# Optimization experiments

Measured on AMD Instinct MI355X. Metric: run time of the kernel, lower is better.

The kernel has to match this reference:

```python
import jax, jax.numpy as jnp
import numpy as np

STRIDE = 16
SIZES = np.array([128.0, 256.0, 512.0], np.float32)
RATIOS = np.array([0.5, 1.0, 2.0], np.float32)
N_POS, N_NEG = 32, 32          # n_sample=64, pos_ratio=0.5
POS_THR, NEG_THR = 0.7, 0.2
W_CONF, W_REG = 1.0, 5.0


def _conv(x, w, b, stride, pad):
    y = jax.lax.conv_general_dilated(x, w, (stride, stride), [(pad, pad), (pad, pad)],
                                     dimension_numbers=('NCHW', 'OIHW', 'NCHW'))
    return y + b[None, :, None, None]


def _anchors(fw, fh, stride):
    # 9 anchors per center: 3 sizes x 3 aspect ratios
    ws = (SIZES[:, None] * np.sqrt(RATIOS)[None, :]).reshape(-1)
    hs = (SIZES[:, None] / np.sqrt(RATIOS)[None, :]).reshape(-1)
    wh = jnp.asarray(np.stack([ws, hs], -1))                      # (9,2)
    cx = (jnp.arange(fw, dtype=jnp.float32) + 0.5) * stride
    cy = (jnp.arange(fh, dtype=jnp.float32) + 0.5) * stride
    gx, gy = jnp.meshgrid(cx, cy, indexing='ij')                  # x-major, like the torch list comp
    ctr = jnp.stack([gx, gy], -1)[:, :, None, :]                  # (fw,fh,1,2)
    tl = ctr - wh / 2.0
    xywh = jnp.concatenate([tl, jnp.broadcast_to(wh, tl.shape)], -1)  # (fw,fh,9,4)
    return xywh.reshape(-1, 4)


def _xywh_to_xyxy(b):
    return jnp.concatenate([b[:, :2], b[:, :2] + b[:, 2:]], -1)


def _iou(a, b):  # a [N,4], b [M,4], xyxy
    lt = jnp.maximum(a[:, None, :2], b[None, :, :2])
    rb = jnp.minimum(a[:, None, 2:], b[None, :, 2:])
    inter = jnp.clip(rb - lt, 0.0).prod(-1)
    aa = (a[:, 2] - a[:, 0]) * (a[:, 3] - a[:, 1])
    ab = (b[:, 2] - b[:, 0]) * (b[:, 3] - b[:, 1])
    return inter / (aa[:, None] + ab[None, :] - inter)


def _head_flat(y, per):  # [1, 9*per, H, W] -> [W*H*9, per], matching anchor flatten order
    _, _, H, W = y.shape
    return y[0].reshape(9, per, H, W).transpose(3, 2, 0, 1).reshape(-1, per)


def _apply_offsets(boxes, off):  # decode proposals from xyxy boxes + (dx,dy,dw,dh)
    w = boxes[:, 2] - boxes[:, 0]; h = boxes[:, 3] - boxes[:, 1]
    cx = boxes[:, 0] + 0.5 * w;    cy = boxes[:, 1] + 0.5 * h
    ncx = cx + off[:, 0] * w;      ncy = cy + off[:, 1] * h
    nw = w * jnp.exp(off[:, 2]);   nh = h * jnp.exp(off[:, 3])
    return jnp.stack([ncx - nw / 2, ncy - nh / 2, ncx + nw / 2, ncy + nh / 2], -1)


def _box_offset(anc, gt):
    aw = anc[:, 2] - anc[:, 0]; ah = anc[:, 3] - anc[:, 1]
    acx = anc[:, 0] + 0.5 * aw; acy = anc[:, 1] + 0.5 * ah
    gw = gt[:, 2] - gt[:, 0];   gh = gt[:, 3] - gt[:, 1]
    gcx = gt[:, 0] + 0.5 * gw;  gcy = gt[:, 1] + 0.5 * gh
    return jnp.stack([(gcx - acx) / aw, (gcy - acy) / ah,
                      jnp.log(gw / aw), jnp.log(gh / ah)], -1)


def setup_inputs():
    key = jax.random.key(0)
    ks = jax.random.split(key, 12)
    img_data = jax.random.normal(ks[0], (1, 3, 1600, 1600), jnp.float32)
    x1 = jax.random.uniform(ks[1], (64,), minval=0.0, maxval=1400.0)
    y1 = jax.random.uniform(ks[2], (64,), minval=0.0, maxval=1400.0)
    bw = jax.random.uniform(ks[3], (64,), minval=32.0, maxval=200.0)
    bh = jax.random.uniform(ks[4], (64,), minval=32.0, maxval=200.0)
    gt_boxes = jnp.stack([x1, y1, x1 + bw, y1 + bh], -1)[None]   # [1,64,4], all valid (no -1 pad)
    gt_classes = jax.random.randint(ks[5], (1, 64), 1, 21, jnp.int32)
    def w(k, shape, fan):
        return jax.random.normal(k, shape, jnp.float32) * np.float32(np.sqrt(2.0 / fan))
    return dict(
        img_data=img_data, gt_boxes=gt_boxes, gt_classes=gt_classes,
        w1=w(ks[6], (64, 3, 7, 7), 3 * 49),      b1=jnp.zeros(64, jnp.float32),
        w2=w(ks[7], (256, 64, 3, 3), 64 * 9),    b2=jnp.zeros(256, jnp.float32),
        w_rpn=w(ks[8], (256, 256, 3, 3), 256 * 9), b_rpn=jnp.zeros(256, jnp.float32),
        w_cls=w(ks[9], (18, 256, 1, 1), 256),    b_cls=jnp.zeros(18, jnp.float32),
        w_reg=w(ks[10], (36, 256, 1, 1), 256),   b_reg=jnp.zeros(36, jnp.float32),
    )


def reference(img_data, gt_boxes, gt_classes, w1, b1, w2, b2, w_rpn, b_rpn, w_cls, b_cls, w_reg, b_reg):
    # --- feature extractor (total stride 16) ---
    fm = jax.nn.relu(_conv(img_data, w1, b1, 4, 3))
    fm = jax.nn.relu(_conv(fm, w2, b2, 4, 1))            # [1,256,100,100]
    H, W = fm.shape[2], fm.shape[3]
    # --- anchors + IoU matching ---
    anchors_xywh = _anchors(W, H, STRIDE)                # [N,4] xywh
    anchors_xyxy = _xywh_to_xyxy(anchors_xywh)
    gt = gt_boxes[0]                                     # [M,4], all valid
    ious = _iou(anchors_xyxy, gt)                        # [N,M]
    N = ious.shape[0]
    gt_max = ious.max(0)                                 # best iou per gt
    is_gt_best = (ious == gt_max[None, :]).any(1)        # torch: where(iou == gt_max)[0]
    anc_argmax = ious.argmax(1)
    anc_max = ious.max(1)
    labels = jnp.full((N,), -1.0, jnp.float32)
    labels = jnp.where(anc_max < NEG_THR, 0.0, labels)
    labels = jnp.where(is_gt_best, 1.0, labels)
    labels = jnp.where(anc_max > POS_THR, 1.0, labels)
    # --- deterministic pos/neg sampling (fixed sizes; replaces randperm subsampling) ---
    idx = jnp.arange(N, dtype=jnp.float32)
    _, pos_index = jax.lax.top_k(jnp.where(labels == 1.0, anc_max, -1.0), N_POS)
    _, neg_index = jax.lax.top_k(jnp.where(labels == 0.0, 1e6 - idx, -1e9), N_NEG)
    bboxes_pos = anchors_xyxy[pos_index]                 # box_convert(xywh->xyxy) of pos anchors
    # --- proposal module (RPN head) ---
    h = jax.nn.relu(_conv(fm, w_rpn, b_rpn, 1, 1))
    cls = _head_flat(_conv(h, w_cls, b_cls, 1, 0), 2)    # [N,2]
    reg = _head_flat(_conv(h, w_reg, b_reg, 1, 0), 4)    # [N,4]
    pos_score = cls[pos_index]
    neg_score = cls[neg_index]
    offset_pos = reg[pos_index]
    proposals = _apply_offsets(bboxes_pos, offset_pos)
    # --- losses ---
    gt_offset = _box_offset(bboxes_pos, gt[anc_argmax[pos_index]])
    logits = jnp.concatenate([pos_score, neg_score], 0)  # [64,2]
    tgt = jnp.concatenate([jnp.ones(N_POS, jnp.int32), jnp.zeros(N_NEG, jnp.int32)])
    logp = jax.nn.log_softmax(logits, -1)
    cls_loss = -logp[jnp.arange(N_POS + N_NEG), tgt].mean()
    d = gt_offset - offset_pos
    ad = jnp.abs(d)
    reg_loss = jnp.where(ad < 1.0, 0.5 * d * d, ad - 0.5).mean()
    total_rpn_loss = W_CONF * cls_loss + W_REG * reg_loss
    gt_cls_pos = gt_classes[0][anc_argmax[pos_index]]
    return (total_rpn_loss, fm, proposals, pos_index, gt_cls_pos)
```

## Files before the change

### kernel.cpp

```cpp
#include <hip/hip_runtime.h>
#include <math.h>


#define CAP 4096

typedef __attribute__((ext_vector_type(8))) short bf16x8;
typedef __attribute__((ext_vector_type(4))) float f32x4;

#define OFF_F1T     0
#define OFF_HBUF    0
#define OFF_FMT     5171328
#define OFF_CPART   6503040
#define OFF_RPART   7223040
#define OFF_WA1     8663040
#define OFF_W9_2    8672448
#define OFF_W9_3    8746176
#define OFF_WTC     9041088
#define OFF_WTG     9045696
#define OFF_AARG    9054912
#define OFF_NEGM    9144912
#define OFF_POSM    9147728
#define OFF_GTMAX   9150544
#define OFF_CANDS   9150688
#define OFF_CANDI   9154784

__device__ __forceinline__ unsigned short f2bf(float f) {
    unsigned int u = __float_as_uint(f);
    u += 0x7fffu + ((u >> 16) & 1u);
    return (unsigned short)(u >> 16);
}

__device__ __forceinline__ void anchor_box(int i, float& x0, float& y0,
                                           float& x1, float& y1, float& area) {
#pragma clang fp contract(off)
    const float sizes[3]  = {128.f, 256.f, 512.f};
    const float ratios[3] = {0.5f, 1.f, 2.f};
    int a = i % 9;
    int q = i / 9;
    int iy = q % 100;
    int ix = q / 100;
    int s = a / 3, r = a % 3;
    float sq = sqrtf(ratios[r]);
    float w = sizes[s] * sq;
    float h = sizes[s] / sq;
    float cx = ((float)ix + 0.5f) * 16.0f;
    float cy = ((float)iy + 0.5f) * 16.0f;
    x0 = cx - w * 0.5f;
    y0 = cy - h * 0.5f;
    x1 = x0 + w;
    y1 = y0 + h;
    area = (x1 - x0) * (y1 - y0);
}

__device__ __forceinline__ float iou_one(float ax0, float ay0, float ax1, float ay1, float aa,
                                         float bx0, float by0, float bx1, float by1, float ab) {
#pragma clang fp contract(off)
    float ltx = fmaxf(ax0, bx0), lty = fmaxf(ay0, by0);
    float rbx = fminf(ax1, bx1), rby = fminf(ay1, by1);
    float iw = fmaxf(rbx - ltx, 0.0f);
    float ih = fmaxf(rby - lty, 0.0f);
    float inter = iw * ih;
    return inter / ((aa + ab) - inter);
}

__global__ __launch_bounds__(256) void setup_kernel(const float* __restrict__ wc, float* __restrict__ wtc,
                                                    const float* __restrict__ wg, float* __restrict__ wtg,
                                                    const float* __restrict__ w1, unsigned short* __restrict__ wa1,
                                                    const float* __restrict__ w2, unsigned short* __restrict__ w9_2,
                                                    const float* __restrict__ wr, unsigned short* __restrict__ w9_3,
                                                    unsigned int* __restrict__ f1t_u, unsigned int* __restrict__ fmt_u,
                                                    unsigned int* __restrict__ gtmax) {
    int i = blockIdx.x * 256 + threadIdx.x;
    if (i < 65) { gtmax[i] = 0u; return; }
    i -= 65;
    if (i < 103040) {
        if (i < 51328) {
            int p = i >> 5, part = i & 31;
            int x, y;
            if (p < 804) { y = (p < 402) ? 0 : 401; x = p % 402; }
            else { int j = p - 804; x = (j < 400) ? 0 : 401; y = 1 + (j % 400); }
            f1t_u[(y * 402 + x) * 32 + part] = 0u;
        } else {
            int i2 = i - 51328;
            int p = i2 >> 7, part = i2 & 127;
            int x, y;
            if (p < 204) { y = (p < 102) ? 0 : 101; x = p % 102; }
            else { int j = p - 204; x = (j < 100) ? 0 : 101; y = 1 + (j % 100); }
            fmt_u[(y * 102 + x) * 128 + part] = 0u;
        }
        return;
    }
    i -= 103040;
    if (i < 4608) { int c = i / 256, k = i - c * 256; wtc[k * 18 + c] = wc[i]; return; }
    i -= 4608;
    if (i < 9216) { int c = i / 256, k = i - c * 256; wtg[k * 36 + c] = wg[i]; return; }
    i -= 9216;
    if (i < 12288) {
        int oc = i / 192, k = i - oc * 192;
        int q = k >> 3, kx = k & 7;
        int ky = q / 3, ic = q - (q / 3) * 3;
        wa1[i] = (q < 21 && kx < 7) ? f2bf(w1[oc * 147 + ic * 49 + ky * 7 + kx])
                                    : (unsigned short)0;
        return;
    }
    i -= 12288;
    if (i < 147456) {
        int cc = i >> 14;
        int rem = i & 16383;
        int ocT = rem >> 10;
        int rem2 = rem & 1023;
        int kcl = rem2 >> 9;
        int lane = (rem2 & 511) >> 3;
        int e = rem2 & 7;
        int oc = ocT * 16 + (lane & 15);
        int ic = kcl * 32 + (lane >> 4) * 8 + e;
        w9_2[i] = f2bf(w2[(oc * 64 + ic) * 9 + cc]);
        return;
    }
    i -= 147456;
    if (i < 589824) {
        int cc = i >> 14;
        int rem = i & 16383;
        int ocT = rem >> 10;
        int rem2 = rem & 1023;
        int kcl = rem2 >> 9;
        int lane = (rem2 & 511) >> 3;
        int e = rem2 & 7;
        int kk = cc >> 2, chv = cc & 3;
        int oc = ocT * 16 + (lane & 15);
        int icl = kcl * 32 + (lane >> 4) * 8 + e;
        w9_3[i] = f2bf(wr[(oc * 256 + chv * 64 + icl) * 9 + kk]);
    }
}

__global__ __launch_bounds__(256) void conv1_mfma(const float* __restrict__ img,
                                                  const unsigned short* __restrict__ wA,
                                                  const float* __restrict__ bias,
                                                  unsigned short* __restrict__ f1t) {
    __shared__ unsigned short win[24 * 260];
    __shared__ unsigned short tileT[64 * 72];
    int t = threadIdx.x;
    int wave = t >> 6, lane = t & 63;
    int quad = lane >> 4, l16 = lane & 15;
    int oy = blockIdx.y;
    int ox0 = blockIdx.x * 64;
    int gx0 = ox0 * 4 - 3;
    int gy0 = 4 * oy - 3;

    int gx = gx0 + t;
    bool xok = (gx >= 0) && (gx < 1600);
    float v[21];
#pragma unroll
    for (int r = 0; r < 21; r++) {
        int ky = r / 3, ic = r - (r / 3) * 3;
        int gy = gy0 + ky;
        v[r] = (xok && gy >= 0 && gy < 1600) ? img[(ic * 1600 + gy) * 1600 + gx] : 0.f;
    }
    float vt = 0.f;
    int rt = t >> 2, ctl = 256 + (t & 3);
    if (rt < 21) {
        int ky = rt / 3, ic = rt - (rt / 3) * 3;
        int gy = gy0 + ky;
        int gxt = gx0 + ctl;
        vt = (gxt >= 0 && gxt < 1600 && gy >= 0 && gy < 1600)
                 ? img[(ic * 1600 + gy) * 1600 + gxt] : 0.f;
    }
    bf16x8 afr[6];
    {
        const bf16x8* ap = (const bf16x8*)(wA + (wave * 16 + l16) * 192 + quad * 8);
#pragma unroll
        for (int c = 0; c < 6; c++) afr[c] = ap[c * 4];
    }
#pragma unroll
    for (int r = 0; r < 21; r++) win[r * 260 + t] = f2bf(v[r]);
    if (rt < 21) win[rt * 260 + ctl] = f2bf(vt);
    win[5460 + t] = 0;
    win[5460 + 256 + t] = 0;
    win[5460 + 512 + t] = 0;
    if (t < 12) win[5460 + 768 + t] = 0;
    __syncthreads();

    f32x4 acc[4];
#pragma unroll
    for (int j = 0; j < 4; j++) acc[j] = (f32x4){0.f, 0.f, 0.f, 0.f};
#pragma unroll
    for (int ch = 0; ch < 6; ch++) {
        const unsigned short* wrow = win + (ch * 4 + quad) * 260;
#pragma unroll
        for (int j = 0; j < 4; j++) {
            int px = j * 16 + l16;
            const unsigned long long* bp = (const unsigned long long*)(wrow + 4 * px);
            union { unsigned long long u[2]; bf16x8 v; } uu;
            uu.u[0] = bp[0];
            uu.u[1] = bp[1];
            acc[j] = __builtin_amdgcn_mfma_f32_16x16x32_bf16(afr[ch], uu.v, acc[j], 0, 0, 0);
        }
    }
#pragma unroll
    for (int reg = 0; reg < 4; reg++) {
        int oc = wave * 16 + quad * 4 + reg;
        float bv = bias[oc];
#pragma unroll
        for (int j = 0; j < 4; j++) {
            int px = j * 16 + l16;
            tileT[px * 72 + oc] = f2bf(fmaxf(acc[j][reg] + bv, 0.f));
        }
    }
    __syncthreads();
    int px = t >> 2, part = t & 3;
    int ox = ox0 + px;
    if (ox < 400) {
        int row = (oy + 1) * 402 + ox + 1;
        uint4 v0 = *(const uint4*)(tileT + px * 72 + part * 16);
        uint4 v1 = *(const uint4*)(tileT + px * 72 + part * 16 + 8);
        *(uint4*)(f1t + row * 64 + part * 16) = v0;
        *(uint4*)(f1t + row * 64 + part * 16 + 8) = v1;
    }
}

template<int ICC, int RS, int S, bool WRT>
__global__ __launch_bounds__(512, 4) void conv_gemm(const unsigned short* __restrict__ Bt,
                                                    const unsigned short* __restrict__ A9,
                                                    const float* __restrict__ bias,
                                                    float* __restrict__ outF,
                                                    unsigned short* __restrict__ outT) {
    const int NC = ICC / 64;
    const int HC = S * 24 + 3;
    const int LROW = ICC + 8;
    const int CHW = ICC / 8;
    const int TOT = 3 * HC * CHW;
    const int NIT = (TOT + 511) / 512;
    __shared__ __align__(16) unsigned short blds[3 * HC * LROW];
    int t = threadIdx.x;
    int xs = blockIdx.x, y = blockIdx.y;

    uint4 stg[NIT];
#pragma unroll
    for (int i = 0; i < NIT; i++) {
        int idx = t + i * 512;
        if (idx < TOT) {
            int row = idx / CHW, e = idx - row * CHW;
            int ky = row / HC, c = row - ky * HC;
            stg[i] = ((const uint4*)(Bt + ((size_t)(S * y + ky) * RS + S * xs * 25 + c) * ICC))[e];
        }
    }
#pragma unroll
    for (int i = 0; i < NIT; i++) {
        int idx = t + i * 512;
        if (idx < TOT) {
            int row = idx / CHW, e = idx - row * CHW;
            int c = row % HC;
            int e2 = (S == 4) ? (e ^ ((c >> 2) & 7)) : e;
            *(uint4*)(blds + row * LROW + e2 * 8) = stg[i];
        }
    }

    int wave = t >> 6, lane = t & 63;
    int ow = wave & 3, kg = wave >> 2;
    int quad = lane >> 4, l16 = lane & 15;
    int oc0 = ow * 64;
    int pxe0 = min(l16, 24);
    int pxe1 = min(16 + l16, 24);
    int sw0 = pxe0 & 7, sw1 = pxe1 & 7;

    f32x4 acc[4][2];
#pragma unroll
    for (int mt = 0; mt < 4; mt++)
#pragma unroll
        for (int j = 0; j < 2; j++) acc[mt][j] = (f32x4){0.f, 0.f, 0.f, 0.f};

    const bf16x8* Av = (const bf16x8*)A9;
    __syncthreads();

    const int CC0 = (NC == 1) ? 0 : kg * 18;
    const int CC1 = (NC == 1) ? 9 : kg * 18 + 18;
    const int KL0 = (NC == 1) ? kg : 0;
    const int KL1 = (NC == 1) ? kg + 1 : 2;

    for (int cc = CC0; cc < CC1; cc++) {
        int pass = cc / NC, ch = cc - pass * NC;
        int ky = pass / 3, kx = pass - (pass / 3) * 3;
        int rb0 = (ky * HC + S * pxe0 + kx) * LROW + ch * 64;
        int rb1 = (ky * HC + S * pxe1 + kx) * LROW + ch * 64;
        for (int kcl = KL0; kcl < KL1; kcl++) {
            bf16x8 af[4];
#pragma unroll
            for (int mt = 0; mt < 4; mt++)
                af[mt] = Av[(size_t)cc * 2048 + (ow * 4 + mt) * 128 + kcl * 64 + lane];
            int ck = kcl * 4 + quad;
            bf16x8 bf0 = *(const bf16x8*)(blds + rb0 + ((S == 4) ? (ck ^ sw0) : ck) * 8);
            bf16x8 bf1 = *(const bf16x8*)(blds + rb1 + ((S == 4) ? (ck ^ sw1) : ck) * 8);
#pragma unroll
            for (int mt = 0; mt < 4; mt++) {
                acc[mt][0] = __builtin_amdgcn_mfma_f32_16x16x32_bf16(af[mt], bf0, acc[mt][0], 0, 0, 0);
                acc[mt][1] = __builtin_amdgcn_mfma_f32_16x16x32_bf16(af[mt], bf1, acc[mt][1], 0, 0, 0);
            }
        }
    }

    __syncthreads();
    float* sred = (float*)blds;
    if (kg == 1) {
#pragma unroll
        for (int mt = 0; mt < 4; mt++)
#pragma unroll
            for (int j = 0; j < 2; j++)
                *(f32x4*)(sred + ((((ow * 4 + mt) * 2 + j) * 64 + lane) * 4)) = acc[mt][j];
    }
    __syncthreads();
    if (kg == 0) {
#pragma unroll
        for (int mt = 0; mt < 4; mt++)
#pragma unroll
            for (int j = 0; j < 2; j++) {
                f32x4 o = *(const f32x4*)(sred + ((((ow * 4 + mt) * 2 + j) * 64 + lane) * 4));
                acc[mt][j] = acc[mt][j] + o;
            }
#pragma unroll
        for (int mt = 0; mt < 4; mt++) {
#pragma unroll
            for (int reg = 0; reg < 4; reg++) {
                int oc = oc0 + mt * 16 + quad * 4 + reg;
                float bv = bias[oc];
#pragma unroll
                for (int j = 0; j < 2; j++) {
                    int pl = j * 16 + l16;
                    if (pl < 25) {
                        int p = y * 100 + xs * 25 + pl;
                        float v = fmaxf(acc[mt][j][reg] + bv, 0.f);
                        outF[oc * 10000 + p] = v;
                        if (WRT) {
                            int r = (y + 1) * 102 + xs * 25 + pl + 1;
                            outT[r * 256 + oc] = f2bf(v);
                        }
                    }
                }
            }
        }
    }
}

__global__ __launch_bounds__(64) void head_kernel(const float* __restrict__ hbuf,
                                                  const float* __restrict__ wtc,
                                                  const float* __restrict__ wtg,
                                                  float* __restrict__ cpart,
                                                  float* __restrict__ rpart) {
    int p = blockIdx.x * 64 + threadIdx.x;
    int ch = blockIdx.y;
    int ic0 = ch * 64;
    if (p >= 10000) return;
    float acc[54];
#pragma unroll
    for (int j = 0; j < 54; j++) acc[j] = 0.f;
    for (int ic = 0; ic < 64; ic += 8) {
        float vv[8];
#pragma unroll
        for (int u = 0; u < 8; u++) vv[u] = hbuf[(ic0 + ic + u) * 10000 + p];
#pragma unroll
        for (int u = 0; u < 8; u++) {
            const float* wc_ = wtc + (ic0 + ic + u) * 18;
#pragma unroll
            for (int j = 0; j < 18; j++) acc[j] += vv[u] * wc_[j];
            const float* wg_ = wtg + (ic0 + ic + u) * 36;
#pragma unroll
            for (int j = 0; j < 36; j++) acc[18 + j] += vv[u] * wg_[j];
        }
    }
    for (int j = 0; j < 18; j++) cpart[(ch * 18 + j) * 10000 + p] = acc[j];
    for (int j = 0; j < 36; j++) rpart[(ch * 36 + j) * 10000 + p] = acc[18 + j];
}

__global__ __launch_bounds__(256) void iou_pass1(const float* __restrict__ gt,
                                                 int* __restrict__ aarg,
                                                 unsigned int* __restrict__ gtmax) {
    __shared__ float sg[64][4];
    __shared__ float sarea[64];
    __shared__ unsigned int smax[64];
    int t = threadIdx.x;
    if (t < 64) {
#pragma clang fp contract(off)
        float b0 = gt[t * 4 + 0], b1 = gt[t * 4 + 1];
        float b2 = gt[t * 4 + 2], b3 = gt[t * 4 + 3];
        sg[t][0] = b0; sg[t][1] = b1; sg[t][2] = b2; sg[t][3] = b3;
        sarea[t] = (b2 - b0) * (b3 - b1);
        smax[t] = 0u;
    }
    __syncthreads();
    int i = blockIdx.x * 256 + t;
    int iq = min(i, 89999);
    float x0, y0, x1, y1, aa;
    anchor_box(iq, x0, y0, x1, y1, aa);
    float best = -1.f;
    int bestj = 0;
    for (int j = 0; j < 64; j++) {
        float v = iou_one(x0, y0, x1, y1, aa, sg[j][0], sg[j][1], sg[j][2], sg[j][3], sarea[j]);
        if (v > best) { best = v; bestj = j; }
        float vm = v;
#pragma unroll
        for (int off = 32; off > 0; off >>= 1) vm = fmaxf(vm, __shfl_xor(vm, off));
        if ((t & 63) == 0) atomicMax(&smax[j], __float_as_uint(vm));
    }
    if (i < 90000) aarg[i] = bestj;
    __syncthreads();
    if (t < 64) atomicMax(&gtmax[t], smax[t]);
}

__global__ __launch_bounds__(256) void iou_pass2(const float* __restrict__ gt,
                                                 const unsigned int* __restrict__ gtmax,
                                                 unsigned long long* __restrict__ negmask,
                                                 unsigned long long* __restrict__ posmask,
                                                 float* __restrict__ cand_s,
                                                 int* __restrict__ cand_i,
                                                 unsigned int* __restrict__ cnt) {
    __shared__ float sg[64][4];
    __shared__ float sarea[64];
    __shared__ float sgm[64];
    int t = threadIdx.x;
    if (t < 64) {
#pragma clang fp contract(off)
        float b0 = gt[t * 4 + 0], b1 = gt[t * 4 + 1];
        float b2 = gt[t * 4 + 2], b3 = gt[t * 4 + 3];
        sg[t][0] = b0; sg[t][1] = b1; sg[t][2] = b2; sg[t][3] = b3;
        sarea[t] = (b2 - b0) * (b3 - b1);
        sgm[t] = __uint_as_float(gtmax[t]);
    }
    __syncthreads();
    int i = blockIdx.x * 256 + t;
    if (i >= 90000) return;
    float x0, y0, x1, y1, aa;
    anchor_box(i, x0, y0, x1, y1, aa);
    float best = -1.f;
    bool isbest = false;
    for (int j = 0; j < 64; j++) {
        float v = iou_one(x0, y0, x1, y1, aa, sg[j][0], sg[j][1], sg[j][2], sg[j][3], sarea[j]);
        if (v > best) best = v;
        if (v == sgm[j]) isbest = true;
    }
    float label = -1.f;
    if (best < 0.2f) label = 0.f;
    if (isbest) label = 1.f;
    if (best > 0.7f) label = 1.f;
    unsigned long long negb = __ballot(label == 0.f);
    unsigned long long posb = __ballot(label == 1.f);
    if ((t & 63) == 0) { negmask[i >> 6] = negb; posmask[i >> 6] = posb; }
    if (label == 1.f) {
        unsigned int p = atomicAdd(cnt, 1u);
        if (p < CAP) { cand_s[p] = best; cand_i[p] = i; }
    }
}

__device__ __forceinline__ unsigned long long shflx64(unsigned long long v, int m) {
    int lo = __shfl_xor((int)(unsigned)(v & 0xFFFFFFFFull), m);
    int hi = __shfl_xor((int)(unsigned)(v >> 32), m);
    return ((unsigned long long)(unsigned)hi << 32) | (unsigned)lo;
}

__device__ int wave_first32(const unsigned long long* __restrict__ mask,
                            bool invert, int* __restrict__ outIdx, int lane) {
    const int NW = 1407;
    const int WPT = 22;
    unsigned long long mw[WPT];
    int cnt = 0;
#pragma unroll
    for (int u = 0; u < WPT; u++) {
        int w = lane * WPT + u;
        unsigned long long m = 0ull;
        if (w < NW) {
            m = mask[w];
            if (invert) m = ~m;
            if (w == NW - 1) m &= 0xFFFFull;
        }
        mw[u] = m;
        cnt += __builtin_popcountll(m);
    }
    int inc = cnt;
#pragma unroll
    for (int off = 1; off < 64; off <<= 1) {
        int v = __shfl_up(inc, off);
        if (lane >= off) inc += v;
    }
    int total = __shfl(inc, 63);
    int pref = inc - cnt;
    if (pref < 32) {
#pragma unroll
        for (int u = 0; u < WPT; u++) {
            unsigned long long m = mw[u];
            int wbase = (lane * WPT + u) * 64;
            while (m && pref < 32) {
                int b = __builtin_ctzll(m);
                outIdx[pref++] = wbase + b;
                m &= m - 1;
            }
        }
    }
    return total;
}

__global__ __launch_bounds__(64) void tail_kernel(const unsigned long long* __restrict__ negmask,
                                                  const unsigned long long* __restrict__ posmask,
                                                  const float* __restrict__ cand_s,
                                                  const int* __restrict__ cand_i,
                                                  const unsigned int* __restrict__ cnt,
                                                  const float* __restrict__ cpart,
                                                  const float* __restrict__ rpart,
                                                  const float* __restrict__ bcls,
                                                  const float* __restrict__ breg,
                                                  const int* __restrict__ aarg,
                                                  const float* __restrict__ gt,
                                                  const int* __restrict__ gtc,
                                                  float* __restrict__ out) {
    __shared__ unsigned long long keys[CAP + 32];
    __shared__ int sfill[32];
    __shared__ int spidx[32];
    __shared__ int snidx[32];
    int lane = threadIdx.x;

    int ncand = min((int)*cnt, CAP);
    for (int c = lane; c < ncand; c += 64) {
        unsigned u = __float_as_uint(cand_s[c]);
        u ^= (u & 0x80000000u) ? 0xFFFFFFFFu : 0x80000000u;
        keys[c] = ((unsigned long long)u << 32) | (0xFFFFFFFFu - (unsigned)cand_i[c]);
    }
    int ntot = ncand;
    if (ncand < 32) {
        int tot = wave_first32(posmask, true, sfill, lane);
        int nfill = min(tot, 32);
        unsigned um1 = __float_as_uint(-1.0f) ^ 0xFFFFFFFFu;
        for (int k2 = lane; k2 < nfill; k2 += 64)
            keys[ncand + k2] = ((unsigned long long)um1 << 32) | (0xFFFFFFFFu - (unsigned)sfill[k2]);
        ntot += nfill;
    }

    unsigned long long lk = 0ull; int ls = -1;
    for (int c = lane; c < ntot; c += 64) {
        unsigned long long k = keys[c];
        if (k > lk) { lk = k; ls = c; }
    }
    for (int s = 0; s < 32; s++) {
        unsigned long long mk = lk;
#pragma unroll
        for (int off = 1; off < 64; off <<= 1) {
            unsigned long long o = shflx64(mk, off);
            if (o > mk) mk = o;
        }
        if (lk == mk && mk != 0ull) {
            spidx[s] = (int)(0xFFFFFFFFu - (unsigned)(mk & 0xFFFFFFFFull));
            keys[ls] = 0ull;
            lk = 0ull; ls = -1;
            for (int c = lane; c < ntot; c += 64) {
                unsigned long long k = keys[c];
                if (k > lk) { lk = k; ls = c; }
            }
        }
    }

    int totn = wave_first32(negmask, false, snidx, lane);
    if (lane == 0) {
        int nf = min(totn, 32);
        for (int s = nf; s < 32; s++) snidx[s] = s;
    }

    {
#pragma clang fp contract(off)
        const int PROP_OFF = 1 + 2560000;
        int t = lane;
        int n = (t < 32) ? spidx[t] : snidx[t - 32];
        int a = n % 9;
        int q = n / 9;
        int iy = q % 100;
        int ix = q / 100;
        int p = iy * 100 + ix;

        float l0 = bcls[a * 2 + 0], l1 = bcls[a * 2 + 1];
        for (int c = 0; c < 4; c++) {
            l0 += cpart[(c * 18 + a * 2 + 0) * 10000 + p];
            l1 += cpart[(c * 18 + a * 2 + 1) * 10000 + p];
        }
        float m = fmaxf(l0, l1);
        float lse = m + logf(expf(l0 - m) + expf(l1 - m));
        float logp = ((t < 32) ? l1 : l0) - lse;
        float cls_sum = logp;
#pragma unroll
        for (int off = 32; off > 0; off >>= 1) cls_sum += __shfl_down(cls_sum, off);

        float reg_sum = 0.f;
        if (t < 32) {
            float offv[4];
#pragma unroll
            for (int k = 0; k < 4; k++) {
                float v = breg[a * 4 + k];
                for (int c = 0; c < 4; c++) v += rpart[(c * 36 + a * 4 + k) * 10000 + p];
                offv[k] = v;
            }
            float x0, y0, x1, y1, aa;
            anchor_box(n, x0, y0, x1, y1, aa);
            float w = x1 - x0, h = y1 - y0;
            float cx = x0 + 0.5f * w, cy = y0 + 0.5f * h;
            float ncx = cx + offv[0] * w, ncy = cy + offv[1] * h;
            float nw = w * expf(offv[2]), nh = h * expf(offv[3]);
            out[PROP_OFF + t * 4 + 0] = ncx - nw * 0.5f;
            out[PROP_OFF + t * 4 + 1] = ncy - nh * 0.5f;
            out[PROP_OFF + t * 4 + 2] = ncx + nw * 0.5f;
            out[PROP_OFF + t * 4 + 3] = ncy + nh * 0.5f;

            int j = aarg[n];
            float g0 = gt[j * 4 + 0], g1 = gt[j * 4 + 1];
            float g2 = gt[j * 4 + 2], g3 = gt[j * 4 + 3];
            float gw = g2 - g0, gh = g3 - g1;
            float gcx = g0 + 0.5f * gw, gcy = g1 + 0.5f * gh;
            float tg[4];
            tg[0] = (gcx - cx) / w;
            tg[1] = (gcy - cy) / h;
            tg[2] = logf(gw / w);
            tg[3] = logf(gh / h);
#pragma unroll
            for (int k = 0; k < 4; k++) {
                float d = tg[k] - offv[k];
                float ad = fabsf(d);
                reg_sum += (ad < 1.f) ? 0.5f * d * d : ad - 0.5f;
            }
            out[PROP_OFF + 128 + t] = (float)n;
            out[PROP_OFF + 160 + t] = (float)gtc[j];
        }
#pragma unroll
        for (int off = 32; off > 0; off >>= 1) reg_sum += __shfl_down(reg_sum, off);
        if (t == 0) {
            float cls_loss = -(cls_sum / 64.f);
            float reg_loss = reg_sum / 128.f;
            out[0] = cls_loss + 5.f * reg_loss;
        }
    }
}

extern "C" void kernel_launch(void* const* d_in, const int* in_sizes, int n_in,
                              void* d_out, int out_size, void* d_ws, size_t ws_size,
                              hipStream_t stream) {
    const float* img = (const float*)d_in[0];
    const float* gt  = (const float*)d_in[1];
    const int*   gtc = (const int*)d_in[2];
    const float* w1  = (const float*)d_in[3];
    const float* b1  = (const float*)d_in[4];
    const float* w2  = (const float*)d_in[5];
    const float* b2  = (const float*)d_in[6];
    const float* wr  = (const float*)d_in[7];
    const float* br  = (const float*)d_in[8];
    const float* wc  = (const float*)d_in[9];
    const float* bc  = (const float*)d_in[10];
    const float* wg  = (const float*)d_in[11];
    const float* bg  = (const float*)d_in[12];
    float* out = (float*)d_out;
    float* ws = (float*)d_ws;

    unsigned short* f1t  = (unsigned short*)(ws + OFF_F1T);
    unsigned short* fmt  = (unsigned short*)(ws + OFF_FMT);
    unsigned short* wa1  = (unsigned short*)(ws + OFF_WA1);
    unsigned short* w9_2 = (unsigned short*)(ws + OFF_W9_2);
    unsigned short* w9_3 = (unsigned short*)(ws + OFF_W9_3);
    float* hbuf  = ws + OFF_HBUF;
    float* cpart = ws + OFF_CPART;
    float* rpart = ws + OFF_RPART;
    float* wtc   = ws + OFF_WTC;
    float* wtg   = ws + OFF_WTG;
    int*   aarg  = (int*)(ws + OFF_AARG);
    unsigned long long* negm = (unsigned long long*)(ws + OFF_NEGM);
    unsigned long long* posm = (unsigned long long*)(ws + OFF_POSM);
    unsigned int* gtmax = (unsigned int*)(ws + OFF_GTMAX);
    unsigned int* cnt   = gtmax + 64;
    float* cands = ws + OFF_CANDS;
    int*   candi = (int*)(ws + OFF_CANDI);
    float* fm    = out + 1;

    setup_kernel<<<dim3(3385), dim3(256), 0, stream>>>(wc, wtc, wg, wtg, w1, wa1,
                                                       w2, w9_2, wr, w9_3,
                                                       (unsigned int*)f1t, (unsigned int*)fmt, gtmax);

    conv1_mfma<<<dim3(7, 400), dim3(256), 0, stream>>>(img, wa1, b1, f1t);
    conv_gemm<64, 402, 4, true><<<dim3(4, 100), dim3(512), 0, stream>>>(f1t, w9_2, b2, fm, fmt);
    conv_gemm<256, 102, 1, false><<<dim3(4, 100), dim3(512), 0, stream>>>(fmt, w9_3, br, hbuf, nullptr);
    head_kernel<<<dim3(157, 4), dim3(64), 0, stream>>>(hbuf, wtc, wtg, cpart, rpart);

    iou_pass1<<<dim3(352), dim3(256), 0, stream>>>(gt, aarg, gtmax);
    iou_pass2<<<dim3(352), dim3(256), 0, stream>>>(gt, gtmax, negm, posm, cands, candi, cnt);
    tail_kernel<<<dim3(1), dim3(64), 0, stream>>>(negm, posm, cands, candi, cnt,
                                                  cpart, rpart, bc, bg, aarg, gt, gtc, out);
}
```

Baseline: 280.6 us.

## Fuse IoU passes into conv kernels and fold RPN head into conv3

The independent IoU labeling passes now run as extra blocks inside the conv1 and conv2 launches, so they share a launch with the convolutions instead of running as separate kernels. The 1x1 cls/reg head is computed inside the conv3 epilogue from an LDS tile, which removes the full-resolution hbuf write and re-read and the separate head launch. The launch count drops from seven to four. The cost is extra shared memory and per-block work in conv3, and heterogeneous blocks within one grid.

```diff
diff --git a/kernel.cpp b/kernel.cpp
--- a/kernel.cpp
+++ b/kernel.cpp
@@ -8,7 +8,6 @@
 typedef __attribute__((ext_vector_type(4))) float f32x4;
 
 #define OFF_F1T     0
-#define OFF_HBUF    0
 #define OFF_FMT     5171328
 #define OFF_CPART   6503040
 #define OFF_RPART   7223040
@@ -133,308 +132,67 @@
     }
 }
 
-__global__ __launch_bounds__(256) void conv1_mfma(const float* __restrict__ img,
-                                                  const unsigned short* __restrict__ wA,
-                                                  const float* __restrict__ bias,
-                                                  unsigned short* __restrict__ f1t) {
-    __shared__ unsigned short win[24 * 260];
-    __shared__ unsigned short tileT[64 * 72];
-    int t = threadIdx.x;
-    int wave = t >> 6, lane = t & 63;
-    int quad = lane >> 4, l16 = lane & 15;
-    int oy = blockIdx.y;
-    int ox0 = blockIdx.x * 64;
-    int gx0 = ox0 * 4 - 3;
-    int gy0 = 4 * oy - 3;
-
-    int gx = gx0 + t;
-    bool xok = (gx >= 0) && (gx < 1600);
-    float v[21];
-#pragma unroll
-    for (int r = 0; r < 21; r++) {
-        int ky = r / 3, ic = r - (r / 3) * 3;
-        int gy = gy0 + ky;
-        v[r] = (xok && gy >= 0 && gy < 1600) ? img[(ic * 1600 + gy) * 1600 + gx] : 0.f;
-    }
-    float vt = 0.f;
-    int rt = t >> 2, ctl = 256 + (t & 3);
-    if (rt < 21) {
-        int ky = rt / 3, ic = rt - (rt / 3) * 3;
-        int gy = gy0 + ky;
-        int gxt = gx0 + ctl;
-        vt = (gxt >= 0 && gxt < 1600 && gy >= 0 && gy < 1600)
-                 ? img[(ic * 1600 + gy) * 1600 + gxt] : 0.f;
-    }
-    bf16x8 afr[6];
-    {
-        const bf16x8* ap = (const bf16x8*)(wA + (wave * 16 + l16) * 192 + quad * 8);
-#pragma unroll
-        for (int c = 0; c < 6; c++) afr[c] = ap[c * 4];
-    }
-#pragma unroll
-    for (int r = 0; r < 21; r++) win[r * 260 + t] = f2bf(v[r]);
-    if (rt < 21) win[rt * 260 + ctl] = f2bf(vt);
-    win[5460 + t] = 0;
-    win[5460 + 256 + t] = 0;
-    win[5460 + 512 + t] = 0;
-    if (t < 12) win[5460 + 768 + t] = 0;
-    __syncthreads();
-
-    f32x4 acc[4];
-#pragma unroll
-    for (int j = 0; j < 4; j++) acc[j] = (f32x4){0.f, 0.f, 0.f, 0.f};
-#pragma unroll
-    for (int ch = 0; ch < 6; ch++) {
-        const unsigned short* wrow = win + (ch * 4 + quad) * 260;
-#pragma unroll
-        for (int j = 0; j < 4; j++) {
-            int px = j * 16 + l16;
-            const unsigned long long* bp = (const unsigned long long*)(wrow + 4 * px);
-            union { unsigned long long u[2]; bf16x8 v; } uu;
-            uu.u[0] = bp[0];
-            uu.u[1] = bp[1];
-            acc[j] = __builtin_amdgcn_mfma_f32_16x16x32_bf16(afr[ch], uu.v, acc[j], 0, 0, 0);
-        }
-    }
-#pragma unroll
-    for (int reg = 0; reg < 4; reg++) {
-        int oc = wave * 16 + quad * 4 + reg;
-        float bv = bias[oc];
-#pragma unroll
-        for (int j = 0; j < 4; j++) {
-            int px = j * 16 + l16;
-            tileT[px * 72 + oc] = f2bf(fmaxf(acc[j][reg] + bv, 0.f));
-        }
-    }
-    __syncthreads();
-    int px = t >> 2, part = t & 3;
-    int ox = ox0 + px;
-    if (ox < 400) {
-        int row = (oy + 1) * 402 + ox + 1;
-        uint4 v0 = *(const uint4*)(tileT + px * 72 + part * 16);
-        uint4 v1 = *(const uint4*)(tileT + px * 72 + part * 16 + 8);
-        *(uint4*)(f1t + row * 64 + part * 16) = v0;
-        *(uint4*)(f1t + row * 64 + part * 16 + 8) = v1;
-    }
-}
-
-template<int ICC, int RS, int S, bool WRT>
-__global__ __launch_bounds__(512, 4) void conv_gemm(const unsigned short* __restrict__ Bt,
-                                                    const unsigned short* __restrict__ A9,
-                                                    const float* __restrict__ bias,
-                                                    float* __restrict__ outF,
-                                                    unsigned short* __restrict__ outT) {
-    const int NC = ICC / 64;
-    const int HC = S * 24 + 3;
-    const int LROW = ICC + 8;
-    const int CHW = ICC / 8;
-    const int TOT = 3 * HC * CHW;
-    const int NIT = (TOT + 511) / 512;
-    __shared__ __align__(16) unsigned short blds[3 * HC * LROW];
-    int t = threadIdx.x;
-    int xs = blockIdx.x, y = blockIdx.y;
-
-    uint4 stg[NIT];
-#pragma unroll
-    for (int i = 0; i < NIT; i++) {
-        int idx = t + i * 512;
-        if (idx < TOT) {
-            int row = idx / CHW, e = idx - row * CHW;
-            int ky = row / HC, c = row - ky * HC;
-            stg[i] = ((const uint4*)(Bt + ((size_t)(S * y + ky) * RS + S * xs * 25 + c) * ICC))[e];
-        }
-    }
-#pragma unroll
-    for (int i = 0; i < NIT; i++) {
-        int idx = t + i * 512;
-        if (idx < TOT) {
-            int row = idx / CHW, e = idx - row * CHW;
-            int c = row % HC;
-            int e2 = (S == 4) ? (e ^ ((c >> 2) & 7)) : e;
-            *(uint4*)(blds + row * LROW + e2 * 8) = stg[i];
-        }
-    }
-
-    int wave = t >> 6, lane = t & 63;
-    int ow = wave & 3, kg = wave >> 2;
-    int quad = lane >> 4, l16 = lane & 15;
-    int oc0 = ow * 64;
-    int pxe0 = min(l16, 24);
-    int pxe1 = min(16 + l16, 24);
-    int sw0 = pxe0 & 7, sw1 = pxe1 & 7;
-
-    f32x4 acc[4][2];
-#pragma unroll
-    for (int mt = 0; mt < 4; mt++)
-#pragma unroll
-        for (int j = 0; j < 2; j++) acc[mt][j] = (f32x4){0.f, 0.f, 0.f, 0.f};
-
-    const bf16x8* Av = (const bf16x8*)A9;
-    __syncthreads();
-
-    const int CC0 = (NC == 1) ? 0 : kg * 18;
-    const int CC1 = (NC == 1) ? 9 : kg * 18 + 18;
-    const int KL0 = (NC == 1) ? kg : 0;
-    const int KL1 = (NC == 1) ? kg + 1 : 2;
-
-    for (int cc = CC0; cc < CC1; cc++) {
-        int pass = cc / NC, ch = cc - pass * NC;
-        int ky = pass / 3, kx = pass - (pass / 3) * 3;
-        int rb0 = (ky * HC + S * pxe0 + kx) * LROW + ch * 64;
-        int rb1 = (ky * HC + S * pxe1 + kx) * LROW + ch * 64;
-        for (int kcl = KL0; kcl < KL1; kcl++) {
-            bf16x8 af[4];
-#pragma unroll
-            for (int mt = 0; mt < 4; mt++)
-                af[mt] = Av[(size_t)cc * 2048 + (ow * 4 + mt) * 128 + kcl * 64 + lane];
-            int ck = kcl * 4 + quad;
-            bf16x8 bf0 = *(const bf16x8*)(blds + rb0 + ((S == 4) ? (ck ^ sw0) : ck) * 8);
-            bf16x8 bf1 = *(const bf16x8*)(blds + rb1 + ((S == 4) ? (ck ^ sw1) : ck) * 8);
-#pragma unroll
-            for (int mt = 0; mt < 4; mt++) {
-                acc[mt][0] = __builtin_amdgcn_mfma_f32_16x16x32_bf16(af[mt], bf0, acc[mt][0], 0, 0, 0);
-                acc[mt][1] = __builtin_amdgcn_mfma_f32_16x16x32_bf16(af[mt], bf1, acc[mt][1], 0, 0, 0);
-            }
-        }
-    }
-
-    __syncthreads();
-    float* sred = (float*)blds;
-    if (kg == 1) {
-#pragma unroll
-        for (int mt = 0; mt < 4; mt++)
-#pragma unroll
-            for (int j = 0; j < 2; j++)
-                *(f32x4*)(sred + ((((ow * 4 + mt) * 2 + j) * 64 + lane) * 4)) = acc[mt][j];
-    }
-    __syncthreads();
-    if (kg == 0) {
-#pragma unroll
-        for (int mt = 0; mt < 4; mt++)
-#pragma unroll
-            for (int j = 0; j < 2; j++) {
-                f32x4 o = *(const f32x4*)(sred + ((((ow * 4 + mt) * 2 + j) * 64 + lane) * 4));
-                acc[mt][j] = acc[mt][j] + o;
-            }
-#pragma unroll
-        for (int mt = 0; mt < 4; mt++) {
-#pragma unroll
-            for (int reg = 0; reg < 4; reg++) {
-                int oc = oc0 + mt * 16 + quad * 4 + reg;
-                float bv = bias[oc];
-#pragma unroll
-                for (int j = 0; j < 2; j++) {
-                    int pl = j * 16 + l16;
-                    if (pl < 25) {
-                        int p = y * 100 + xs * 25 + pl;
-                        float v = fmaxf(acc[mt][j][reg] + bv, 0.f);
-                        outF[oc * 10000 + p] = v;
-                        if (WRT) {
-                            int r = (y + 1) * 102 + xs * 25 + pl + 1;
-                            outT[r * 256 + oc] = f2bf(v);
-                        }
-                    }
-                }
-            }
-        }
-    }
-}
-
-__global__ __launch_bounds__(64) void head_kernel(const float* __restrict__ hbuf,
-                                                  const float* __restrict__ wtc,
-                                                  const float* __restrict__ wtg,
-                                                  float* __restrict__ cpart,
-                                                  float* __restrict__ rpart) {
-    int p = blockIdx.x * 64 + threadIdx.x;
-    int ch = blockIdx.y;
-    int ic0 = ch * 64;
-    if (p >= 10000) return;
-    float acc[54];
-#pragma unroll
-    for (int j = 0; j < 54; j++) acc[j] = 0.f;
-    for (int ic = 0; ic < 64; ic += 8) {
-        float vv[8];
-#pragma unroll
-        for (int u = 0; u < 8; u++) vv[u] = hbuf[(ic0 + ic + u) * 10000 + p];
-#pragma unroll
-        for (int u = 0; u < 8; u++) {
-            const float* wc_ = wtc + (ic0 + ic + u) * 18;
-#pragma unroll
-            for (int j = 0; j < 18; j++) acc[j] += vv[u] * wc_[j];
-            const float* wg_ = wtg + (ic0 + ic + u) * 36;
-#pragma unroll
-            for (int j = 0; j < 36; j++) acc[18 + j] += vv[u] * wg_[j];
-        }
-    }
-    for (int j = 0; j < 18; j++) cpart[(ch * 18 + j) * 10000 + p] = acc[j];
-    for (int j = 0; j < 36; j++) rpart[(ch * 36 + j) * 10000 + p] = acc[18 + j];
-}
-
-__global__ __launch_bounds__(256) void iou_pass1(const float* __restrict__ gt,
-                                                 int* __restrict__ aarg,
-                                                 unsigned int* __restrict__ gtmax) {
-    __shared__ float sg[64][4];
-    __shared__ float sarea[64];
-    __shared__ unsigned int smax[64];
-    int t = threadIdx.x;
+__device__ __forceinline__ void iou1_body(int bid, int t, const float* __restrict__ gt,
+                                          int* __restrict__ aarg, unsigned int* __restrict__ gtmax) {
+    __shared__ float sg1[64][4];
+    __shared__ float sarea1[64];
+    __shared__ unsigned int smax1[64];
     if (t < 64) {
 #pragma clang fp contract(off)
         float b0 = gt[t * 4 + 0], b1 = gt[t * 4 + 1];
         float b2 = gt[t * 4 + 2], b3 = gt[t * 4 + 3];
-        sg[t][0] = b0; sg[t][1] = b1; sg[t][2] = b2; sg[t][3] = b3;
-        sarea[t] = (b2 - b0) * (b3 - b1);
-        smax[t] = 0u;
+        sg1[t][0] = b0; sg1[t][1] = b1; sg1[t][2] = b2; sg1[t][3] = b3;
+        sarea1[t] = (b2 - b0) * (b3 - b1);
+        smax1[t] = 0u;
     }
     __syncthreads();
-    int i = blockIdx.x * 256 + t;
+    int i = bid * 256 + t;
     int iq = min(i, 89999);
     float x0, y0, x1, y1, aa;
     anchor_box(iq, x0, y0, x1, y1, aa);
     float best = -1.f;
     int bestj = 0;
     for (int j = 0; j < 64; j++) {
-        float v = iou_one(x0, y0, x1, y1, aa, sg[j][0], sg[j][1], sg[j][2], sg[j][3], sarea[j]);
+        float v = iou_one(x0, y0, x1, y1, aa, sg1[j][0], sg1[j][1], sg1[j][2], sg1[j][3], sarea1[j]);
         if (v > best) { best = v; bestj = j; }
         float vm = v;
 #pragma unroll
         for (int off = 32; off > 0; off >>= 1) vm = fmaxf(vm, __shfl_xor(vm, off));
-        if ((t & 63) == 0) atomicMax(&smax[j], __float_as_uint(vm));
+        if ((t & 63) == 0) atomicMax(&smax1[j], __float_as_uint(vm));
     }
     if (i < 90000) aarg[i] = bestj;
     __syncthreads();
-    if (t < 64) atomicMax(&gtmax[t], smax[t]);
-}
-
-__global__ __launch_bounds__(256) void iou_pass2(const float* __restrict__ gt,
-                                                 const unsigned int* __restrict__ gtmax,
-                                                 unsigned long long* __restrict__ negmask,
-                                                 unsigned long long* __restrict__ posmask,
-                                                 float* __restrict__ cand_s,
-                                                 int* __restrict__ cand_i,
-                                                 unsigned int* __restrict__ cnt) {
-    __shared__ float sg[64][4];
-    __shared__ float sarea[64];
-    __shared__ float sgm[64];
-    int t = threadIdx.x;
+    if (t < 64) atomicMax(&gtmax[t], smax1[t]);
+}
+
+__device__ __forceinline__ void iou2_body(int bid, int t, const float* __restrict__ gt,
+                                          const unsigned int* __restrict__ gtmax,
+                                          unsigned long long* __restrict__ negmask,
+                                          unsigned long long* __restrict__ posmask,
+                                          float* __restrict__ cand_s, int* __restrict__ cand_i,
+                                          unsigned int* __restrict__ cnt) {
+    __shared__ float sg2[64][4];
+    __shared__ float sarea2[64];
+    __shared__ float sgm2[64];
     if (t < 64) {
 #pragma clang fp contract(off)
         float b0 = gt[t * 4 + 0], b1 = gt[t * 4 + 1];
         float b2 = gt[t * 4 + 2], b3 = gt[t * 4 + 3];
-        sg[t][0] = b0; sg[t][1] = b1; sg[t][2] = b2; sg[t][3] = b3;
-        sarea[t] = (b2 - b0) * (b3 - b1);
-        sgm[t] = __uint_as_float(gtmax[t]);
+        sg2[t][0] = b0; sg2[t][1] = b1; sg2[t][2] = b2; sg2[t][3] = b3;
+        sarea2[t] = (b2 - b0) * (b3 - b1);
+        sgm2[t] = __uint_as_float(gtmax[t]);
     }
     __syncthreads();
-    int i = blockIdx.x * 256 + t;
+    int i = bid * 512 + t;
     if (i >= 90000) return;
     float x0, y0, x1, y1, aa;
     anchor_box(i, x0, y0, x1, y1, aa);
     float best = -1.f;
     bool isbest = false;
     for (int j = 0; j < 64; j++) {
-        float v = iou_one(x0, y0, x1, y1, aa, sg[j][0], sg[j][1], sg[j][2], sg[j][3], sarea[j]);
+        float v = iou_one(x0, y0, x1, y1, aa, sg2[j][0], sg2[j][1], sg2[j][2], sg2[j][3], sarea2[j]);
         if (v > best) best = v;
-        if (v == sgm[j]) isbest = true;
+        if (v == sgm2[j]) isbest = true;
     }
     float label = -1.f;
     if (best < 0.2f) label = 0.f;
@@ -447,6 +205,294 @@
         unsigned int p = atomicAdd(cnt, 1u);
         if (p < CAP) { cand_s[p] = best; cand_i[p] = i; }
     }
+}
+
+__device__ __forceinline__ void conv1_body(int bx, int oy, int t,
+                                           const float* __restrict__ img,
+                                           const unsigned short* __restrict__ wA,
+                                           const float* __restrict__ bias,
+                                           unsigned short* __restrict__ f1t) {
+    __shared__ unsigned short win[24 * 260];
+    __shared__ unsigned short tileT[64 * 72];
+    int wave = t >> 6, lane = t & 63;
+    int quad = lane >> 4, l16 = lane & 15;
+    int ox0 = bx * 64;
+    int gx0 = ox0 * 4 - 3;
+    int gy0 = 4 * oy - 3;
+
+    int gx = gx0 + t;
+    bool xok = (gx >= 0) && (gx < 1600);
+    float v[21];
+#pragma unroll
+    for (int r = 0; r < 21; r++) {
+        int ky = r / 3, ic = r - (r / 3) * 3;
+        int gy = gy0 + ky;
+        v[r] = (xok && gy >= 0 && gy < 1600) ? img[(ic * 1600 + gy) * 1600 + gx] : 0.f;
+    }
+    float vt = 0.f;
+    int rt = t >> 2, ctl = 256 + (t & 3);
+    if (rt < 21) {
+        int ky = rt / 3, ic = rt - (rt / 3) * 3;
+        int gy = gy0 + ky;
+        int gxt = gx0 + ctl;
+        vt = (gxt >= 0 && gxt < 1600 && gy >= 0 && gy < 1600)
+                 ? img[(ic * 1600 + gy) * 1600 + gxt] : 0.f;
+    }
+    bf16x8 afr[6];
+    {
+        const bf16x8* ap = (const bf16x8*)(wA + (wave * 16 + l16) * 192 + quad * 8);
+#pragma unroll
+        for (int c = 0; c < 6; c++) afr[c] = ap[c * 4];
+    }
+#pragma unroll
+    for (int r = 0; r < 21; r++) win[r * 260 + t] = f2bf(v[r]);
+    if (rt < 21) win[rt * 260 + ctl] = f2bf(vt);
+    win[5460 + t] = 0;
+    win[5460 + 256 + t] = 0;
+    win[5460 + 512 + t] = 0;
+    if (t < 12) win[5460 + 768 + t] = 0;
+    __syncthreads();
+
+    f32x4 acc[4];
+#pragma unroll
+    for (int j = 0; j < 4; j++) acc[j] = (f32x4){0.f, 0.f, 0.f, 0.f};
+#pragma unroll
+    for (int ch = 0; ch < 6; ch++) {
+        const unsigned short* wrow = win + (ch * 4 + quad) * 260;
+#pragma unroll
+        for (int j = 0; j < 4; j++) {
+            int px = j * 16 + l16;
+            const unsigned long long* bp = (const unsigned long long*)(wrow + 4 * px);
+            union { unsigned long long u[2]; bf16x8 v; } uu;
+            uu.u[0] = bp[0];
+            uu.u[1] = bp[1];
+            acc[j] = __builtin_amdgcn_mfma_f32_16x16x32_bf16(afr[ch], uu.v, acc[j], 0, 0, 0);
+        }
+    }
+#pragma unroll
+    for (int reg = 0; reg < 4; reg++) {
+        int oc = wave * 16 + quad * 4 + reg;
+        float bv = bias[oc];
+#pragma unroll
+        for (int j = 0; j < 4; j++) {
+            int px = j * 16 + l16;
+            tileT[px * 72 + oc] = f2bf(fmaxf(acc[j][reg] + bv, 0.f));
+        }
+    }
+    __syncthreads();
+    int px = t >> 2, part = t & 3;
+    int ox = ox0 + px;
+    if (ox < 400) {
+        int row = (oy + 1) * 402 + ox + 1;
+        uint4 v0 = *(const uint4*)(tileT + px * 72 + part * 16);
+        uint4 v1 = *(const uint4*)(tileT + px * 72 + part * 16 + 8);
+        *(uint4*)(f1t + row * 64 + part * 16) = v0;
+        *(uint4*)(f1t + row * 64 + part * 16 + 8) = v1;
+    }
+}
+
+__global__ __launch_bounds__(256) void conv1_iou1(const float* __restrict__ img,
+                                                  const unsigned short* __restrict__ wA,
+                                                  const float* __restrict__ bias,
+                                                  unsigned short* __restrict__ f1t,
+                                                  const float* __restrict__ gt,
+                                                  int* __restrict__ aarg,
+                                                  unsigned int* __restrict__ gtmax) {
+    int t = threadIdx.x;
+    if (blockIdx.x < 7) {
+        conv1_body(blockIdx.x, blockIdx.y, t, img, wA, bias, f1t);
+    } else {
+        int bid = blockIdx.y;
+        if (bid < 352) iou1_body(bid, t, gt, aarg, gtmax);
+    }
+}
+
+template<int ICC, int RS, int S, bool WRT, bool HEAD>
+__device__ __forceinline__ void conv_body(int xs, int y, int t,
+                                          const unsigned short* __restrict__ Bt,
+                                          const unsigned short* __restrict__ A9,
+                                          const float* __restrict__ bias,
+                                          float* __restrict__ outF,
+                                          unsigned short* __restrict__ outT,
+                                          const float* __restrict__ wtc,
+                                          const float* __restrict__ wtg,
+                                          float* __restrict__ cpart,
+                                          float* __restrict__ rpart) {
+    constexpr int NC = ICC / 64;
+    constexpr int HC = S * 24 + 3;
+    constexpr int LROW = ICC + 8;
+    constexpr int CHW = ICC / 8;
+    constexpr int TOT = 3 * HC * CHW;
+    constexpr int NIT = (TOT + 511) / 512;
+    constexpr int BB = 3 * HC * LROW * 2;
+    constexpr int SMB = HEAD ? (32768 + 256 * 26 * 4) : BB;
+    static_assert(BB <= 61440, "B tile too big");
+    __shared__ __align__(16) unsigned char smem[SMB];
+    unsigned short* blds = (unsigned short*)smem;
+    float* sred = (float*)smem;
+    float* hlds = (float*)(smem + 32768);
+
+    uint4 stg[NIT];
+#pragma unroll
+    for (int i = 0; i < NIT; i++) {
+        int idx = t + i * 512;
+        if (idx < TOT) {
+            int row = idx / CHW, e = idx - row * CHW;
+            int ky = row / HC, c = row - ky * HC;
+            stg[i] = ((const uint4*)(Bt + ((size_t)(S * y + ky) * RS + S * xs * 25 + c) * ICC))[e];
+        }
+    }
+#pragma unroll
+    for (int i = 0; i < NIT; i++) {
+        int idx = t + i * 512;
+        if (idx < TOT) {
+            int row = idx / CHW, e = idx - row * CHW;
+            int c = row % HC;
+            int e2 = (S == 4) ? (e ^ ((c >> 2) & 7)) : e;
+            *(uint4*)(blds + row * LROW + e2 * 8) = stg[i];
+        }
+    }
+
+    int wave = t >> 6, lane = t & 63;
+    int ow = wave & 3, kg = wave >> 2;
+    int quad = lane >> 4, l16 = lane & 15;
+    int oc0 = ow * 64;
+    int pxe0 = min(l16, 24);
+    int pxe1 = min(16 + l16, 24);
+    int sw0 = pxe0 & 7, sw1 = pxe1 & 7;
+
+    f32x4 acc[4][2];
+#pragma unroll
+    for (int mt = 0; mt < 4; mt++)
+#pragma unroll
+        for (int j = 0; j < 2; j++) acc[mt][j] = (f32x4){0.f, 0.f, 0.f, 0.f};
+
+    const bf16x8* Av = (const bf16x8*)A9;
+    __syncthreads();
+
+    const int CC0 = (NC == 1) ? 0 : kg * 18;
+    const int CC1 = (NC == 1) ? 9 : kg * 18 + 18;
+    const int KL0 = (NC == 1) ? kg : 0;
+    const int KL1 = (NC == 1) ? kg + 1 : 2;
+
+    for (int cc = CC0; cc < CC1; cc++) {
+        int pass = cc / NC, ch = cc - pass * NC;
+        int ky = pass / 3, kx = pass - (pass / 3) * 3;
+        int rb0 = (ky * HC + S * pxe0 + kx) * LROW + ch * 64;
+        int rb1 = (ky * HC + S * pxe1 + kx) * LROW + ch * 64;
+        for (int kcl = KL0; kcl < KL1; kcl++) {
+            bf16x8 af[4];
+#pragma unroll
+            for (int mt = 0; mt < 4; mt++)
+                af[mt] = Av[(size_t)cc * 2048 + (ow * 4 + mt) * 128 + kcl * 64 + lane];
+            int ck = kcl * 4 + quad;
+            bf16x8 bf0 = *(const bf16x8*)(blds + rb0 + ((S == 4) ? (ck ^ sw0) : ck) * 8);
+            bf16x8 bf1 = *(const bf16x8*)(blds + rb1 + ((S == 4) ? (ck ^ sw1) : ck) * 8);
+#pragma unroll
+            for (int mt = 0; mt < 4; mt++) {
+                acc[mt][0] = __builtin_amdgcn_mfma_f32_16x16x32_bf16(af[mt], bf0, acc[mt][0], 0, 0, 0);
+                acc[mt][1] = __builtin_amdgcn_mfma_f32_16x16x32_bf16(af[mt], bf1, acc[mt][1], 0, 0, 0);
+            }
+        }
+    }
+
+    __syncthreads();
+    if (kg == 1) {
+#pragma unroll
+        for (int mt = 0; mt < 4; mt++)
+#pragma unroll
+            for (int j = 0; j < 2; j++)
+                *(f32x4*)(sred + ((((ow * 4 + mt) * 2 + j) * 64 + lane) * 4)) = acc[mt][j];
+    }
+    __syncthreads();
+    if (kg == 0) {
+#pragma unroll
+        for (int mt = 0; mt < 4; mt++)
+#pragma unroll
+            for (int j = 0; j < 2; j++) {
+                f32x4 o = *(const f32x4*)(sred + ((((ow * 4 + mt) * 2 + j) * 64 + lane) * 4));
+                acc[mt][j] = acc[mt][j] + o;
+            }
+#pragma unroll
+        for (int mt = 0; mt < 4; mt++) {
+#pragma unroll
+            for (int reg = 0; reg < 4; reg++) {
+                int oc = oc0 + mt * 16 + quad * 4 + reg;
+                float bv = bias[oc];
+#pragma unroll
+                for (int j = 0; j < 2; j++) {
+                    int pl = j * 16 + l16;
+                    if (pl < 25) {
+                        float v = fmaxf(acc[mt][j][reg] + bv, 0.f);
+                        if (HEAD) {
+                            hlds[oc * 26 + pl] = v;
+                        } else {
+                            int p = y * 100 + xs * 25 + pl;
+                            outF[oc * 10000 + p] = v;
+                            if (WRT) {
+                                int r = (y + 1) * 102 + xs * 25 + pl + 1;
+                                outT[r * 256 + oc] = f2bf(v);
+                            }
+                        }
+                    }
+                }
+            }
+        }
+    }
+    if (HEAD) {
+        __syncthreads();
+        int base = y * 100 + xs * 25;
+        for (int it = t; it < 5400; it += 512) {
+            int ch = it / 1350;
+            int r = it - ch * 1350;
+            int j = r / 25;
+            int p = r - j * 25;
+            int jc = (j < 18) ? j : (j - 18);
+            const float* wt = (j < 18) ? (wtc + jc) : (wtg + jc);
+            int stride = (j < 18) ? 18 : 36;
+            int ic0 = ch * 64;
+            float acc2 = 0.f;
+#pragma unroll 8
+            for (int ic = 0; ic < 64; ic++)
+                acc2 += hlds[(ic0 + ic) * 26 + p] * wt[(ic0 + ic) * stride];
+            float* dst = (j < 18) ? (cpart + (ch * 18 + jc) * 10000)
+                                  : (rpart + (ch * 36 + jc) * 10000);
+            dst[base + p] = acc2;
+        }
+    }
+}
+
+__global__ __launch_bounds__(512, 4) void conv2_iou2(const unsigned short* __restrict__ Bt,
+                                                     const unsigned short* __restrict__ A9,
+                                                     const float* __restrict__ bias,
+                                                     float* __restrict__ outF,
+                                                     unsigned short* __restrict__ outT,
+                                                     const float* __restrict__ gt,
+                                                     const unsigned int* __restrict__ gtmax,
+                                                     unsigned long long* __restrict__ negmask,
+                                                     unsigned long long* __restrict__ posmask,
+                                                     float* __restrict__ cand_s,
+                                                     int* __restrict__ cand_i,
+                                                     unsigned int* __restrict__ cnt) {
+    int t = threadIdx.x;
+    if (blockIdx.x < 4) {
+        conv_body<64, 402, 4, true, false>(blockIdx.x, blockIdx.y, t, Bt, A9, bias,
+                                           outF, outT, nullptr, nullptr, nullptr, nullptr);
+    } else {
+        int bid = (blockIdx.x - 4) * 100 + blockIdx.y;
+        if (bid < 176) iou2_body(bid, t, gt, gtmax, negmask, posmask, cand_s, cand_i, cnt);
+    }
+}
+
+__global__ __launch_bounds__(512, 4) void conv3_head(const unsigned short* __restrict__ Bt,
+                                                     const unsigned short* __restrict__ A9,
+                                                     const float* __restrict__ bias,
+                                                     const float* __restrict__ wtc,
+                                                     const float* __restrict__ wtg,
+                                                     float* __restrict__ cpart,
+                                                     float* __restrict__ rpart) {
+    conv_body<256, 102, 1, false, true>(blockIdx.x, blockIdx.y, threadIdx.x, Bt, A9, bias,
+                                        nullptr, nullptr, wtc, wtg, cpart, rpart);
 }
 
 __device__ __forceinline__ unsigned long long shflx64(unsigned long long v, int m) {
@@ -656,7 +702,6 @@
     unsigned short* wa1  = (unsigned short*)(ws + OFF_WA1);
     unsigned short* w9_2 = (unsigned short*)(ws + OFF_W9_2);
     unsigned short* w9_3 = (unsigned short*)(ws + OFF_W9_3);
-    float* hbuf  = ws + OFF_HBUF;
     float* cpart = ws + OFF_CPART;
     float* rpart = ws + OFF_RPART;
     float* wtc   = ws + OFF_WTC;
@@ -674,13 +719,10 @@
                                                        w2, w9_2, wr, w9_3,
                                                        (unsigned int*)f1t, (unsigned int*)fmt, gtmax);
 
-    conv1_mfma<<<dim3(7, 400), dim3(256), 0, stream>>>(img, wa1, b1, f1t);
-    conv_gemm<64, 402, 4, true><<<dim3(4, 100), dim3(512), 0, stream>>>(f1t, w9_2, b2, fm, fmt);
-    conv_gemm<256, 102, 1, false><<<dim3(4, 100), dim3(512), 0, stream>>>(fmt, w9_3, br, hbuf, nullptr);
-    head_kernel<<<dim3(157, 4), dim3(64), 0, stream>>>(hbuf, wtc, wtg, cpart, rpart);
-
-    iou_pass1<<<dim3(352), dim3(256), 0, stream>>>(gt, aarg, gtmax);
-    iou_pass2<<<dim3(352), dim3(256), 0, stream>>>(gt, gtmax, negm, posm, cands, candi, cnt);
+    conv1_iou1<<<dim3(8, 400), dim3(256), 0, stream>>>(img, wa1, b1, f1t, gt, aarg, gtmax);
+    conv2_iou2<<<dim3(6, 100), dim3(512), 0, stream>>>(f1t, w9_2, b2, fm, fmt,
+                                                       gt, gtmax, negm, posm, cands, candi, cnt);
+    conv3_head<<<dim3(4, 100), dim3(512), 0, stream>>>(fmt, w9_3, br, wtc, wtg, cpart, rpart);
     tail_kernel<<<dim3(1), dim3(64), 0, stream>>>(negm, posm, cands, candi, cnt,
                                                   cpart, rpart, bc, bg, aarg, gt, gtc, out);
 }
```

Measured after the change: 275.3 us. About the same (-1.9%).
